# Kernel tuning notes

Measured on AMD Instinct MI355X. Metric: run time of the kernel, lower is better.

## Reference

```python
import jax, jax.numpy as jnp
import numpy as np

N, M, D = 16384, 4096, 128
NEG = -1e30  # masked-score fill


def setup_inputs() -> dict:
    key = jax.random.key(0)
    k1, k2, k3, k4 = jax.random.split(key, 4)
    self_feats = jax.random.normal(k1, (N, D), dtype=jnp.float32)
    features_neighs = jax.random.normal(k2, (M, D), dtype=jnp.float32)
    neigh_matrix = jax.random.randint(k3, (N, M), 0, 2, dtype=jnp.int32)
    # xavier_uniform for a: shape (2D, 1), gain=1 -> limit = sqrt(6/(2D+1))
    limit = float(np.sqrt(6.0 / (2 * D + 1)))
    a = jax.random.uniform(k4, (2 * D, 1), minval=-limit, maxval=limit, dtype=jnp.float32)
    return {"self_feats": self_feats, "features_neighs": features_neighs,
            "neigh_matrix": neigh_matrix, "a": a}


def reference(self_feats, features_neighs, neigh_matrix, a):
    # a = [a_self; a_neigh]; cat([self_i, neigh_j]) @ a = self_i@a_self + neigh_j@a_neigh
    d = self_feats.shape[1]
    s_self = self_feats @ a[:d, 0]        # [N]
    s_neigh = features_neighs @ a[d:, 0]  # [M]
    scores = jax.nn.leaky_relu(s_self[:, None] + s_neigh[None, :], 0.2)  # [N, M]
    mask = neigh_matrix.astype(bool)
    scores = jnp.where(mask, scores, NEG)
    attn = jax.nn.softmax(scores, axis=1)          # masked softmax per node
    attn = jnp.where(mask, attn, 0.0)              # nodes with no neighbors -> zeros
    return attn @ features_neighs                  # [N, D] weighted neighbor sum
```

## Files before the change

### kernel.cpp

```cpp
#include <hip/hip_runtime.h>
#include <hip/hip_bf16.h>

#define NROWS 16384
#define MCOLS 4096
#define DDIM  128
#define LOG2E 1.4426950408889634f

typedef __attribute__((ext_vector_type(8))) short short8;
typedef __attribute__((ext_vector_type(4))) float f32x4;

__device__ __forceinline__ float wave_reduce_add(float d) {
#pragma unroll
  for (int off = 32; off >= 1; off >>= 1) d += __shfl_xor(d, off, 64);
  return d;
}

__device__ __forceinline__ float pcalc(float t, int m) {
  float u = fmaxf(t, 0.2f * t);
  float e = exp2f(u);
  return m != 0 ? e : 0.f;
}

__device__ __forceinline__ unsigned short f2bf(float f) {
  unsigned u = __builtin_bit_cast(unsigned, f);
  return (unsigned short)((u + 0x7fffu + ((u >> 16) & 1u)) >> 16);
}

__device__ __forceinline__ unsigned pack_bf2(float lo, float hi) {
  return (unsigned)f2bf(lo) | ((unsigned)f2bf(hi) << 16);
}

__global__ __launch_bounds__(256) void aggr_prep(
    const float* __restrict__ V, const float* __restrict__ a,
    float* __restrict__ sneigh, short* __restrict__ packedV) {
  const int t = threadIdx.x, lane = t & 63, w = t >> 6;
  const int blk = blockIdx.x;

  float a0 = a[DDIM + 2 * lane] * LOG2E;
  float a1 = a[DDIM + 2 * lane + 1] * LOG2E;
#pragma unroll
  for (int i = 0; i < 4; ++i) {
    int j = blk * 16 + w * 4 + i;
    float2 v = *(const float2*)(V + (long)j * DDIM + 2 * lane);
    float d = wave_reduce_add(v.x * a0 + v.y * a1);
    if (lane == 0) sneigh[j] = d;
  }

  const int tg = blk * 256 + t;
  const int l = tg & 63;
  const int chunkid = tg >> 6;
  const int c = chunkid & 15, kt = chunkid >> 4;
  const int ks2 = c >> 3, cf = c & 7;
  const int col = cf * 16 + (l & 15);
  const long krow = (long)kt * 64 + ks2 * 32 + (l >> 4) * 8;
  short8 o;
#pragma unroll
  for (int b = 0; b < 8; ++b) {
    float f = V[(krow + b) * DDIM + col];
    o[b] = (short)f2bf(f);
  }
  *(short8*)(packedV + (long)tg * 8) = o;
}

#define BODY(I, SC, BUF, STG, MSK, VMC)                                        \
  {                                                                            \
    const int i_ = (I);                                                        \
    if (STG) STAGE((BUF) ^ 1, i_ + 1);                                         \
    __builtin_amdgcn_sched_barrier(0);                                         \
    if (MSK) MASK((((SC) + 3) & 3), i_ + 3);                                   \
    __builtin_amdgcn_sched_barrier(0);                                         \
    short8 afr[2];                                                             \
    _Pragma("unroll")                                                          \
    for (int ks2 = 0; ks2 < 2; ++ks2) {                                        \
      const float* sj = &s_sn[(ks * 32 + i_) * 64 + ks2 * 32 + kg * 8];        \
      float4 s0 = *(const float4*)sj;                                          \
      float4 s1 = *(const float4*)(sj + 4);                                    \
      int4 m0 = rg[SC][ks2 * 2], m1 = rg[SC][ks2 * 2 + 1];                     \
      float p0 = pcalc(si + s0.x, m0.x);                                       \
      float p1 = pcalc(si + s0.y, m0.y);                                       \
      float p2 = pcalc(si + s0.z, m0.z);                                       \
      float p3 = pcalc(si + s0.w, m0.w);                                       \
      float p4 = pcalc(si + s1.x, m1.x);                                       \
      float p5 = pcalc(si + s1.y, m1.y);                                       \
      float p6 = pcalc(si + s1.z, m1.z);                                       \
      float p7 = pcalc(si + s1.w, m1.w);                                       \
      den += ((p0 + p1) + (p2 + p3)) + ((p4 + p5) + (p6 + p7));                \
      int4 ai;                                                                 \
      ai.x = (int)pack_bf2(p0, p1);                                            \
      ai.y = (int)pack_bf2(p2, p3);                                            \
      ai.z = (int)pack_bf2(p4, p5);                                            \
      ai.w = (int)pack_bf2(p6, p7);                                            \
      afr[ks2] = __builtin_bit_cast(short8, ai);                               \
    }                                                                          \
    const short8* Bks = (const short8*)&Bst[BUF][ks][0];                       \
    _Pragma("unroll")                                                          \
    for (int cf = 0; cf < 8; ++cf) {                                           \
      acc[cf] = __builtin_amdgcn_mfma_f32_16x16x32_bf16(                       \
          afr[0], Bks[cf * 64 + lane], acc[cf], 0, 0, 0);                      \
      acc[cf] = __builtin_amdgcn_mfma_f32_16x16x32_bf16(                       \
          afr[1], Bks[(8 + cf) * 64 + lane], acc[cf], 0, 0, 0);                \
    }                                                                          \
    asm volatile("s_waitcnt vmcnt(" #VMC ")" ::: "memory");                    \
    __builtin_amdgcn_sched_barrier(0);                                         \
    __builtin_amdgcn_s_barrier();                                              \
    __builtin_amdgcn_sched_barrier(0);                                         \
  }

__global__ __launch_bounds__(256, 2) void aggr_main(
    const float* __restrict__ self_feats, const int* __restrict__ nm,
    const float* __restrict__ a, const float* __restrict__ sneigh,
    const short* __restrict__ packedV, float* __restrict__ out) {
  __shared__ float s_sn[MCOLS];
  __shared__ __align__(16) short Bst[2][2][8192];

  const int t = threadIdx.x, lane = t & 63, w = t >> 6;
  const int rw = w & 1, ks = w >> 1;
  const int rowblk = blockIdx.x * 32;
  const int arow = lane & 15, kg = lane >> 4;
  const int row = rowblk + rw * 16 + arow;

  float sip = 0.f;
  {
    const float* rp = self_feats + (long)row * DDIM + kg * 32;
    const float* ap = a + kg * 32;
#pragma unroll
    for (int j = 0; j < 8; ++j) {
      float4 v = *(const float4*)(rp + j * 4);
      float4 av = *(const float4*)(ap + j * 4);
      sip += v.x * av.x + v.y * av.y + v.z * av.z + v.w * av.w;
    }
  }
  sip += __shfl_xor(sip, 16, 64);
  sip += __shfl_xor(sip, 32, 64);
  const float si = sip * LOG2E;

  {
    const float4* src = (const float4*)sneigh;
    float4* dst = (float4*)s_sn;
#pragma unroll
    for (int j = 0; j < 4; ++j) dst[t + j * 256] = src[t + j * 256];
  }

  auto STAGE = [&](int buf, int i) {
    int kt = ks * 32 + i;
#pragma unroll
    for (int j = 0; j < 8; ++j) {
      int c = rw * 8 + j;
      const short* g = packedV + ((long)(kt * 16 + c) * 64 + lane) * 8;
      __builtin_amdgcn_global_load_lds(
          (const __attribute__((address_space(1))) void*)g,
          (__attribute__((address_space(3))) void*)(&Bst[buf][ks][c * 512]),
          16, 0, 0);
    }
  };

  const int* mbase = nm + (long)row * MCOLS + ks * 2048 + kg * 8;
  int4 rg[4][4];
  auto MASK = [&](int slot, int i) {
#pragma unroll
    for (int ks2 = 0; ks2 < 2; ++ks2)
#pragma unroll
      for (int q = 0; q < 2; ++q)
        rg[slot][ks2 * 2 + q] = *(const int4*)(mbase + i * 64 + ks2 * 32 + q * 4);
  };

  __builtin_amdgcn_sched_barrier(0);
  STAGE(0, 0);
  MASK(0, 0);
  MASK(1, 1);
  MASK(2, 2);
  __builtin_amdgcn_sched_barrier(0);
  asm volatile("s_waitcnt vmcnt(12)" ::: "memory");
  __syncthreads();
  asm volatile("s_waitcnt vmcnt(8)" ::: "memory");

  f32x4 acc[8];
#pragma unroll
  for (int i = 0; i < 8; ++i) acc[i] = (f32x4){0.f, 0.f, 0.f, 0.f};
  float den = 0.f;

  for (int it = 0; it < 28; it += 4) {
    BODY(it + 0, 0, 0, true, true, 4)
    BODY(it + 1, 1, 1, true, true, 4)
    BODY(it + 2, 2, 0, true, true, 4)
    BODY(it + 3, 3, 1, true, true, 4)
  }
  BODY(28, 0, 0, true, true, 4)
  BODY(29, 1, 1, true, false, 0)
  BODY(30, 2, 0, true, false, 0)
  BODY(31, 3, 1, false, false, 0)
  __syncthreads();

  den += __shfl_xor(den, 16, 64);
  den += __shfl_xor(den, 32, 64);

  float* comb = (float*)&Bst[0][0][0];
  float* den_x = comb + 32 * 132;
  if (ks == 1) {
#pragma unroll
    for (int cf = 0; cf < 8; ++cf)
#pragma unroll
      for (int r = 0; r < 4; ++r)
        comb[(rw * 16 + kg * 4 + r) * 132 + cf * 16 + arow] = acc[cf][r];
    if (lane < 16) den_x[rw * 16 + lane] = den;
  }
  __syncthreads();
  if (ks == 0) {
    float dtot = den + den_x[rw * 16 + arow];
    float rcp[4];
#pragma unroll
    for (int r = 0; r < 4; ++r) {
      float dv = __shfl(dtot, kg * 4 + r, 64);
      rcp[r] = dv > 0.f ? 1.0f / dv : 0.f;
    }
#pragma unroll
    for (int cf = 0; cf < 8; ++cf)
#pragma unroll
      for (int r = 0; r < 4; ++r)
        out[(long)(rowblk + rw * 16 + kg * 4 + r) * DDIM + cf * 16 + arow] =
            (acc[cf][r] + comb[(rw * 16 + kg * 4 + r) * 132 + cf * 16 + arow]) *
            rcp[r];
  }
}

extern "C" void kernel_launch(void* const* d_in, const int* in_sizes, int n_in,
                              void* d_out, int out_size, void* d_ws, size_t ws_size,
                              hipStream_t stream) {
  const float* self_feats = (const float*)d_in[0];
  const float* V = (const float*)d_in[1];
  const int* nm = (const int*)d_in[2];
  const float* a = (const float*)d_in[3];
  float* out = (float*)d_out;

  float* sneigh = (float*)d_ws;
  short* packedV = (short*)((char*)d_ws + 16384);

  aggr_prep<<<256, 256, 0, stream>>>(V, a, sneigh, packedV);
  aggr_main<<<512, 256, 0, stream>>>(self_feats, nm, a, sneigh, packedV, out);
}
```

Before: 389.7 us.

## Load V fragments directly into registers and drop LDS staging barriers

Replaces the LDS staging of packed V tiles (global_load_lds plus per-iteration barriers) with direct per-wave global loads into a double-buffered register array. Blocks shrink to two waves covering 16 rows, doubling the grid. This removes the per-step workgroup barriers and LDS traffic, at the cost of each wave re-reading V from cache instead of sharing it, and much higher register usage.

```diff
diff --git a/kernel.cpp b/kernel.cpp
--- a/kernel.cpp
+++ b/kernel.cpp
@@ -62,20 +62,34 @@
   *(short8*)(packedV + (long)tg * 8) = o;
 }
 
-#define BODY(I, SC, BUF, STG, MSK, VMC)                                        \
+#define LOADB(BUF_, I_)                                                        \
+  {                                                                            \
+    const short8* g_ =                                                         \
+        (const short8*)packedV + (long)(ks * 32 + (I_)) * 1024 + lane;         \
+    _Pragma("unroll") for (int c = 0; c < 16; ++c) Bfr[BUF_][c] = g_[c * 64];  \
+  }
+
+#define LOADM(S_, I_)                                                          \
+  {                                                                            \
+    _Pragma("unroll") for (int ks2 = 0; ks2 < 2; ++ks2)                        \
+        _Pragma("unroll") for (int q = 0; q < 2; ++q)                          \
+            rg[S_][ks2 * 2 + q] =                                              \
+        *(const int4*)(mbase + (I_)*64 + ks2 * 32 + q * 4);                    \
+  }
+
+#define BODY(I, MS, MLS, BUF)                                                  \
   {                                                                            \
     const int i_ = (I);                                                        \
-    if (STG) STAGE((BUF) ^ 1, i_ + 1);                                         \
+    if (i_ < 31) LOADB((BUF) ^ 1, i_ + 1);                                     \
     __builtin_amdgcn_sched_barrier(0);                                         \
-    if (MSK) MASK((((SC) + 3) & 3), i_ + 3);                                   \
+    if (i_ < 29) LOADM(MLS, i_ + 3);                                           \
     __builtin_amdgcn_sched_barrier(0);                                         \
     short8 afr[2];                                                             \
-    _Pragma("unroll")                                                          \
-    for (int ks2 = 0; ks2 < 2; ++ks2) {                                        \
+    _Pragma("unroll") for (int ks2 = 0; ks2 < 2; ++ks2) {                      \
       const float* sj = &s_sn[(ks * 32 + i_) * 64 + ks2 * 32 + kg * 8];        \
       float4 s0 = *(const float4*)sj;                                          \
       float4 s1 = *(const float4*)(sj + 4);                                    \
-      int4 m0 = rg[SC][ks2 * 2], m1 = rg[SC][ks2 * 2 + 1];                     \
+      int4 m0 = rg[MS][ks2 * 2], m1 = rg[MS][ks2 * 2 + 1];                     \
       float p0 = pcalc(si + s0.x, m0.x);                                       \
       float p1 = pcalc(si + s0.y, m0.y);                                       \
       float p2 = pcalc(si + s0.z, m0.z);                                       \
@@ -92,32 +106,33 @@
       ai.w = (int)pack_bf2(p6, p7);                                            \
       afr[ks2] = __builtin_bit_cast(short8, ai);                               \
     }                                                                          \
-    const short8* Bks = (const short8*)&Bst[BUF][ks][0];                       \
-    _Pragma("unroll")                                                          \
-    for (int cf = 0; cf < 8; ++cf) {                                           \
+    _Pragma("unroll") for (int cf = 0; cf < 8; ++cf) {                         \
       acc[cf] = __builtin_amdgcn_mfma_f32_16x16x32_bf16(                       \
-          afr[0], Bks[cf * 64 + lane], acc[cf], 0, 0, 0);                      \
+          afr[0], Bfr[BUF][cf], acc[cf], 0, 0, 0);                             \
       acc[cf] = __builtin_amdgcn_mfma_f32_16x16x32_bf16(                       \
-          afr[1], Bks[(8 + cf) * 64 + lane], acc[cf], 0, 0, 0);                \
+          afr[1], Bfr[BUF][8 + cf], acc[cf], 0, 0, 0);                         \
     }                                                                          \
-    asm volatile("s_waitcnt vmcnt(" #VMC ")" ::: "memory");                    \
-    __builtin_amdgcn_sched_barrier(0);                                         \
-    __builtin_amdgcn_s_barrier();                                              \
-    __builtin_amdgcn_sched_barrier(0);                                         \
-  }
-
-__global__ __launch_bounds__(256, 2) void aggr_main(
+  }
+
+__global__ __launch_bounds__(128, 2) void aggr_main(
     const float* __restrict__ self_feats, const int* __restrict__ nm,
     const float* __restrict__ a, const float* __restrict__ sneigh,
     const short* __restrict__ packedV, float* __restrict__ out) {
   __shared__ float s_sn[MCOLS];
-  __shared__ __align__(16) short Bst[2][2][8192];
-
-  const int t = threadIdx.x, lane = t & 63, w = t >> 6;
-  const int rw = w & 1, ks = w >> 1;
-  const int rowblk = blockIdx.x * 32;
+
+  const int t = threadIdx.x, lane = t & 63, ks = t >> 6;
+  const int rowblk = blockIdx.x * 16;
   const int arow = lane & 15, kg = lane >> 4;
-  const int row = rowblk + rw * 16 + arow;
+  const int row = rowblk + arow;
+
+  short8 Bfr[2][16];
+  int4 rg[4][4];
+  const int* mbase = nm + (long)row * MCOLS + ks * 2048 + kg * 8;
+
+  LOADB(0, 0)
+  LOADM(0, 0)
+  LOADM(1, 1)
+  LOADM(2, 2)
 
   float sip = 0.f;
   {
@@ -138,75 +153,39 @@
     const float4* src = (const float4*)sneigh;
     float4* dst = (float4*)s_sn;
 #pragma unroll
-    for (int j = 0; j < 4; ++j) dst[t + j * 256] = src[t + j * 256];
-  }
-
-  auto STAGE = [&](int buf, int i) {
-    int kt = ks * 32 + i;
-#pragma unroll
-    for (int j = 0; j < 8; ++j) {
-      int c = rw * 8 + j;
-      const short* g = packedV + ((long)(kt * 16 + c) * 64 + lane) * 8;
-      __builtin_amdgcn_global_load_lds(
-          (const __attribute__((address_space(1))) void*)g,
-          (__attribute__((address_space(3))) void*)(&Bst[buf][ks][c * 512]),
-          16, 0, 0);
-    }
-  };
-
-  const int* mbase = nm + (long)row * MCOLS + ks * 2048 + kg * 8;
-  int4 rg[4][4];
-  auto MASK = [&](int slot, int i) {
-#pragma unroll
-    for (int ks2 = 0; ks2 < 2; ++ks2)
-#pragma unroll
-      for (int q = 0; q < 2; ++q)
-        rg[slot][ks2 * 2 + q] = *(const int4*)(mbase + i * 64 + ks2 * 32 + q * 4);
-  };
-
-  __builtin_amdgcn_sched_barrier(0);
-  STAGE(0, 0);
-  MASK(0, 0);
-  MASK(1, 1);
-  MASK(2, 2);
-  __builtin_amdgcn_sched_barrier(0);
-  asm volatile("s_waitcnt vmcnt(12)" ::: "memory");
+    for (int j = 0; j < 8; ++j) dst[t + j * 128] = src[t + j * 128];
+  }
   __syncthreads();
-  asm volatile("s_waitcnt vmcnt(8)" ::: "memory");
 
   f32x4 acc[8];
 #pragma unroll
   for (int i = 0; i < 8; ++i) acc[i] = (f32x4){0.f, 0.f, 0.f, 0.f};
   float den = 0.f;
 
-  for (int it = 0; it < 28; it += 4) {
-    BODY(it + 0, 0, 0, true, true, 4)
-    BODY(it + 1, 1, 1, true, true, 4)
-    BODY(it + 2, 2, 0, true, true, 4)
-    BODY(it + 3, 3, 1, true, true, 4)
-  }
-  BODY(28, 0, 0, true, true, 4)
-  BODY(29, 1, 1, true, false, 0)
-  BODY(30, 2, 0, true, false, 0)
-  BODY(31, 3, 1, false, false, 0)
-  __syncthreads();
+  for (int it = 0; it < 32; it += 4) {
+    BODY(it + 0, 0, 3, 0)
+    BODY(it + 1, 1, 0, 1)
+    BODY(it + 2, 2, 1, 0)
+    BODY(it + 3, 3, 2, 1)
+  }
 
   den += __shfl_xor(den, 16, 64);
   den += __shfl_xor(den, 32, 64);
 
-  float* comb = (float*)&Bst[0][0][0];
-  float* den_x = comb + 32 * 132;
+  __syncthreads();
+  float* comb = s_sn;
+  float* den_x = s_sn + 2200;
   if (ks == 1) {
 #pragma unroll
     for (int cf = 0; cf < 8; ++cf)
 #pragma unroll
       for (int r = 0; r < 4; ++r)
-        comb[(rw * 16 + kg * 4 + r) * 132 + cf * 16 + arow] = acc[cf][r];
-    if (lane < 16) den_x[rw * 16 + lane] = den;
+        comb[(kg * 4 + r) * 132 + cf * 16 + arow] = acc[cf][r];
+    if (lane < 16) den_x[lane] = den;
   }
   __syncthreads();
   if (ks == 0) {
-    float dtot = den + den_x[rw * 16 + arow];
+    float dtot = den + den_x[arow];
     float rcp[4];
 #pragma unroll
     for (int r = 0; r < 4; ++r) {
@@ -217,9 +196,8 @@
     for (int cf = 0; cf < 8; ++cf)
 #pragma unroll
       for (int r = 0; r < 4; ++r)
-        out[(long)(rowblk + rw * 16 + kg * 4 + r) * DDIM + cf * 16 + arow] =
-            (acc[cf][r] + comb[(rw * 16 + kg * 4 + r) * 132 + cf * 16 + arow]) *
-            rcp[r];
+        out[(long)(rowblk + kg * 4 + r) * DDIM + cf * 16 + arow] =
+            (acc[cf][r] + comb[(kg * 4 + r) * 132 + cf * 16 + arow]) * rcp[r];
   }
 }
 
@@ -236,5 +214,5 @@
   short* packedV = (short*)((char*)d_ws + 16384);
 
   aggr_prep<<<256, 256, 0, stream>>>(V, a, sneigh, packedV);
-  aggr_main<<<512, 256, 0, stream>>>(self_feats, nm, a, sneigh, packedV, out);
-}
+  aggr_main<<<1024, 128, 0, stream>>>(self_feats, nm, a, sneigh, packedV, out);
+}
```

New measurement: 538.8 us. 1.38x slower.
